# Optimization experiments

Hardware: AMD Instinct MI355X
Metric: run time of the kernel (lower is better)

Reference implementation:

```python
import jax, jax.numpy as jnp
import numpy as np

D_MODEL = 1024
N_HEADS = 16
HEAD_DIM = D_MODEL // N_HEADS
SCALE = HEAD_DIM ** -0.5
NEG = -9e15


def setup_inputs() -> dict:
    key = jax.random.key(0)
    k1, k2, k3 = jax.random.split(key, 3)
    B, S = 4, 2048
    x = jax.random.normal(k1, (B, S, D_MODEL), dtype=jnp.float32)
    W_qkv = jax.random.normal(k2, (D_MODEL, 3 * D_MODEL), dtype=jnp.float32) * (D_MODEL ** -0.5)
    b_qkv = jnp.zeros((3 * D_MODEL,), dtype=jnp.float32)
    W_out = jax.random.normal(k3, (D_MODEL, D_MODEL), dtype=jnp.float32) * (D_MODEL ** -0.5)
    b_out = jnp.zeros((D_MODEL,), dtype=jnp.float32)
    return {"x": x, "W_qkv": W_qkv, "b_qkv": b_qkv, "W_out": W_out, "b_out": b_out}


def reference(x, W_qkv, b_qkv, W_out, b_out):
    B, S, _ = x.shape
    qkv = x @ W_qkv + b_qkv                      # [B,S,3D]
    q, k, v = jnp.split(qkv, 3, axis=-1)
    def heads(t):
        return t.reshape(B, S, N_HEADS, HEAD_DIM).transpose(0, 2, 1, 3)  # [B,H,S,d]
    q, k, v = heads(q), heads(k), heads(v)
    logits = jnp.einsum('bhqd,bhkd->bhqk', q, k) * SCALE
    causal = jnp.tril(jnp.ones((S, S), dtype=bool))
    logits = jnp.where(causal[None, None], logits, jnp.float32(NEG))
    attn = jax.nn.softmax(logits, axis=-1)       # dropout p=0 -> identity
    vals = jnp.einsum('bhqk,bhkd->bhqd', attn, v)
    vals = vals.transpose(0, 2, 1, 3).reshape(B, S, D_MODEL)
    return vals @ W_out + b_out
```

## Files before the change

kernel.cpp:

```cpp
#include <hip/hip_runtime.h>

typedef unsigned short u16;
typedef unsigned int u32;
typedef __attribute__((ext_vector_type(8))) short bf16x8;
typedef __attribute__((ext_vector_type(4))) float f32x4;

#define MFMA16(a, b, c) __builtin_amdgcn_mfma_f32_16x16x32_bf16((a), (b), (c), 0, 0, 0)

constexpr int D = 1024;
constexpr int NH = 16;
constexpr int HD = 64;
constexpr int BB = 4;
constexpr int SS = 2048;
constexpr int BH = BB * NH;
constexpr int MTOK = BB * SS;
constexpr float SCALE_LOG2E = 0.125f * 1.44269504088896340736f;

__device__ __forceinline__ u16 f32_bf16(float f) {
  union { float f; u32 u; } v; v.f = f;
  u32 u = v.u;
  u += 0x7FFFu + ((u >> 16) & 1u);
  return (u16)(u >> 16);
}

__device__ __forceinline__ float exp2_fast(float x) {
  float r; asm("v_exp_f32 %0, %1" : "=v"(r) : "v"(x)); return r;
}
__device__ __forceinline__ u16 cvt_bf16_1(float f) {
  u32 r; asm("v_cvt_pk_bf16_f32 %0, %1, %1" : "=v"(r) : "v"(f)); return (u16)r;
}

__device__ __forceinline__ void gload_lds16(const void* g, u16* l) {
  __builtin_amdgcn_global_load_lds(
      (const __attribute__((address_space(1))) u32*)g,
      (__attribute__((address_space(3))) u32*)l, 16, 0, 0);
}

__global__ __launch_bounds__(256)
void cvt_bf16(const float* __restrict__ in, u16* __restrict__ out, int n4) {
  int i = blockIdx.x * 256 + threadIdx.x;
  const int stride = gridDim.x * 256;
  for (; i < n4; i += stride) {
    float4 v = reinterpret_cast<const float4*>(in)[i];
    u32 lo = (u32)f32_bf16(v.x) | ((u32)f32_bf16(v.y) << 16);
    u32 hi = (u32)f32_bf16(v.z) | ((u32)f32_bf16(v.w) << 16);
    reinterpret_cast<uint2*>(out)[i] = make_uint2(lo, hi);
  }
}

__global__ __launch_bounds__(256)
void transpose_bf16(const float* __restrict__ in, u16* __restrict__ out, int R, int C) {
  __shared__ float tile[32][33];
  const int c0 = blockIdx.x * 32, r0 = blockIdx.y * 32;
  const int tx = threadIdx.x, ty = threadIdx.y;
#pragma unroll
  for (int i = 0; i < 4; i++)
    tile[ty + 8 * i][tx] = in[(size_t)(r0 + ty + 8 * i) * C + c0 + tx];
  __syncthreads();
#pragma unroll
  for (int i = 0; i < 4; i++)
    out[(size_t)(c0 + ty + 8 * i) * R + r0 + tx] = f32_bf16(tile[tx][ty + 8 * i]);
}

template <int MODE>
__global__ __launch_bounds__(256)
void gemm_bf16(const u16* __restrict__ A, const u16* __restrict__ Bt,
               const float* __restrict__ bias,
               u16* __restrict__ q_out, u16* __restrict__ k_out,
               u16* __restrict__ vt_out, float* __restrict__ f_out,
               int M, int N, int K) {
  constexpr int BK = 32;
  __shared__ u16 lds_a[128 * BK];
  __shared__ u16 lds_b[128 * BK];
  const int m0 = blockIdx.x * 128;
  const int n0 = blockIdx.y * 128;
  const int t = threadIdx.x;
  const int lane = t & 63;
  const int w = t >> 6;
  const int wr = w >> 1, wc = w & 1;
  const int fr = lane & 15, fq = lane >> 4;

  const int srow = t >> 2;
  const int schunk = (t & 3) ^ ((srow >> 1) & 3);
  const u16* ga0 = A + (size_t)(m0 + srow) * K + schunk * 8;
  const u16* ga1 = ga0 + (size_t)64 * K;
  const u16* gb0 = Bt + (size_t)(n0 + srow) * K + schunk * 8;
  const u16* gb1 = gb0 + (size_t)64 * K;
  u16* la0 = lds_a + t * 8;
  u16* la1 = lds_a + (t + 256) * 8;
  u16* lb0 = lds_b + t * 8;
  u16* lb1 = lds_b + (t + 256) * 8;

  const int swz = ((fr >> 1) & 3) << 4;
  const char* ca = (const char*)lds_a;
  const char* cb = (const char*)lds_b;

  f32x4 acc[4][4] = {};

  for (int k0 = 0; k0 < K; k0 += BK) {
    __syncthreads();
    gload_lds16(ga0, la0);
    gload_lds16(ga1, la1);
    gload_lds16(gb0, lb0);
    gload_lds16(gb1, lb1);
    ga0 += BK; ga1 += BK; gb0 += BK; gb1 += BK;
    __syncthreads();
    bf16x8 af[4], bfr[4];
#pragma unroll
    for (int i = 0; i < 4; i++)
      af[i] = *reinterpret_cast<const bf16x8*>(
          ca + (wr * 64 + i * 16 + fr) * 64 + ((fq * 16) ^ swz));
#pragma unroll
    for (int i = 0; i < 4; i++)
      bfr[i] = *reinterpret_cast<const bf16x8*>(
          cb + (wc * 64 + i * 16 + fr) * 64 + ((fq * 16) ^ swz));
#pragma unroll
    for (int i = 0; i < 4; i++)
#pragma unroll
      for (int j = 0; j < 4; j++)
        acc[i][j] = MFMA16(af[i], bfr[j], acc[i][j]);
  }

#pragma unroll
  for (int i = 0; i < 4; i++) {
#pragma unroll
    for (int j = 0; j < 4; j++) {
      const int ncol = n0 + wc * 64 + j * 16 + fr;
      const float bs = bias[ncol];
#pragma unroll
      for (int r = 0; r < 4; r++) {
        const int mrow = m0 + wr * 64 + i * 16 + fq * 4 + r;
        const float vv = acc[i][j][r] + bs;
        if (MODE == 0) {
          const int which = ncol >> 10;
          const int rem = ncol & 1023;
          const int hh = rem >> 6, dd = rem & 63;
          const int bb = mrow >> 11, ss = mrow & 2047;
          const int bh = bb * 16 + hh;
          if (which == 0)
            q_out[((size_t)bh * SS + ss) * HD + dd] = f32_bf16(vv * SCALE_LOG2E);
          else if (which == 1)
            k_out[((size_t)bh * SS + ss) * HD + dd] = f32_bf16(vv);
          else
            vt_out[((size_t)bh * HD + dd) * SS + ss] = f32_bf16(vv);
        } else {
          f_out[(size_t)mrow * N + ncol] = vv;
        }
      }
    }
  }
}

__global__ __launch_bounds__(512)
void attn_fwd(const u16* __restrict__ Qb, const u16* __restrict__ Kb,
              const u16* __restrict__ Vt, u16* __restrict__ vals) {
  const int bid = blockIdx.x;
  const int wk = (bid & 7) * 64 + (bid >> 3);
  const int bh = wk >> 3;
  const int pA = wk & 7;
  const int qtA = pA, qtB = 15 - pA;
  const int nA = 2 * qtA + 2;
  const int nTot = 34;
  const u16* Qp = Qb + (size_t)bh * SS * HD;
  const char* Kp = (const char*)(Kb + (size_t)bh * SS * HD);
  const char* Vp = (const char*)(Vt + (size_t)bh * HD * SS);
  const int t = threadIdx.x, lane = t & 63, w = t >> 6;
  const int fr = lane & 15, fq = lane >> 4;
  const int swz = (fr & 7) << 4;

  __shared__ u16 kbuf[3][4096];
  __shared__ u16 vbuf[3][4096];
  __shared__ u16 plds[8][16][72];
  u16* myp = &plds[w][0][0];

  const int lin = t * 16;

  int offKV[8];
#pragma unroll
  for (int kf = 0; kf < 4; kf++)
#pragma unroll
    for (int kk = 0; kk < 2; kk++)
      offKV[kf * 2 + kk] = (kf * 16 + fr) * 128 + ((kk * 64 + fq * 16) ^ swz);

  bf16x8 aq[2];
  {
    const int qbase = qtA * 128 + w * 16;
#pragma unroll
    for (int kk = 0; kk < 2; kk++)
      aq[kk] = *reinterpret_cast<const bf16x8*>(Qp + (size_t)(qbase + fr) * HD + kk * 32 + fq * 8);
  }

  f32x4 o[4] = {};
  float mrun[4], lpart[4];
#pragma unroll
  for (int j = 0; j < 4; j++) { mrun[j] = -3e38f; lpart[j] = 0.f; }

#define STAGE(bufi, kvt_)                                                     \
  {                                                                           \
    const int row = lin >> 7, colb = lin & 127;                               \
    const int scol = colb ^ ((row & 7) << 4);                                 \
    gload_lds16(Kp + (size_t)((kvt_) * 64 + row) * 128 + scol,                \
                &kbuf[bufi][lin >> 1]);                                       \
    gload_lds16(Vp + (size_t)row * 4096 + (kvt_) * 128 + scol,                \
                &vbuf[bufi][lin >> 1]);                                       \
  }
#define KVIDX(ti_) ((ti_) >= nA ? (ti_) - nA : (ti_))

  auto write_out = [&](int qt) {
    const int b_ = bh >> 4, h_ = bh & 15;
    const int qb = qt * 128 + w * 16;
    float linv[4];
#pragma unroll
    for (int j = 0; j < 4; j++) {
      float rs = lpart[j];
#pragma unroll
      for (int off = 1; off < 16; off <<= 1)
        rs += __shfl_xor(rs, off, 64);
      linv[j] = 1.f / rs;
    }
#pragma unroll
    for (int df = 0; df < 4; df++)
#pragma unroll
      for (int j = 0; j < 4; j++) {
        const float vv = o[df][j] * linv[j];
        const int qg = qb + fq * 4 + j;
        vals[((size_t)(b_ * SS + qg)) * D + h_ * HD + df * 16 + fr] = cvt_bf16_1(vv);
      }
  };

  int cur = 0;
  STAGE(0, 0);
  STAGE(1, 1);

  for (int ti = 0; ti < nTot; ++ti) {
    const bool segB = ti >= nA;
    const int kvt = segB ? ti - nA : ti;
    const int qt = segB ? qtB : qtA;

    if (ti + 1 < nTot)
      asm volatile("s_waitcnt vmcnt(2)" ::: "memory");
    else
      asm volatile("s_waitcnt vmcnt(0)" ::: "memory");
    __builtin_amdgcn_s_barrier();
    __builtin_amdgcn_sched_barrier(0);

    if (ti == nA) {
      write_out(qtA);
      const int qbase = qtB * 128 + w * 16;
#pragma unroll
      for (int kk = 0; kk < 2; kk++)
        aq[kk] = *reinterpret_cast<const bf16x8*>(Qp + (size_t)(qbase + fr) * HD + kk * 32 + fq * 8);
#pragma unroll
      for (int j = 0; j < 4; j++) { mrun[j] = -3e38f; lpart[j] = 0.f; }
#pragma unroll
      for (int df = 0; df < 4; df++) o[df] = f32x4{0.f, 0.f, 0.f, 0.f};
    }

    const char* kb = (const char*)kbuf[cur];
    const char* vb = (const char*)vbuf[cur];

    f32x4 sc[4] = {};
    __builtin_amdgcn_s_setprio(1);
#pragma unroll
    for (int kf = 0; kf < 4; kf++) {
#pragma unroll
      for (int kk = 0; kk < 2; kk++) {
        bf16x8 bk = *reinterpret_cast<const bf16x8*>(kb + offKV[kf * 2 + kk]);
        sc[kf] = MFMA16(aq[kk], bk, sc[kf]);
      }
    }
    __builtin_amdgcn_s_setprio(0);
    if ((kvt >> 1) == qt) {
      const int kg0 = kvt * 64 + fr;
      const int rg0 = qt * 128 + w * 16 + fq * 4;
#pragma unroll
      for (int kf = 0; kf < 4; kf++)
#pragma unroll
        for (int j = 0; j < 4; j++)
          if (kg0 + kf * 16 > rg0 + j) sc[kf][j] = -3e38f;
    }
    float mj[4];
#pragma unroll
    for (int j = 0; j < 4; j++) {
      float m = fmaxf(fmaxf(sc[0][j], sc[1][j]), fmaxf(sc[2][j], sc[3][j]));
#pragma unroll
      for (int off = 1; off < 16; off <<= 1)
        m = fmaxf(m, __shfl_xor(m, off, 64));
      mj[j] = m;
    }
    const bool need = (mj[0] > mrun[0] + 8.f) | (mj[1] > mrun[1] + 8.f) |
                      (mj[2] > mrun[2] + 8.f) | (mj[3] > mrun[3] + 8.f);
    if (__any((int)need)) {
#pragma unroll
      for (int j = 0; j < 4; j++) {
        const float mnew = fmaxf(mrun[j], mj[j]);
        const float alpha = exp2_fast(mrun[j] - mnew);
        mrun[j] = mnew;
        lpart[j] *= alpha;
#pragma unroll
        for (int df = 0; df < 4; df++) o[df][j] *= alpha;
      }
    }
#pragma unroll
    for (int j = 0; j < 4; j++) {
#pragma unroll
      for (int kf = 0; kf < 4; kf++) {
        const float p = exp2_fast(sc[kf][j] - mrun[j]);
        sc[kf][j] = p;
        lpart[j] += p;
      }
    }
#pragma unroll
    for (int kf = 0; kf < 4; kf++)
#pragma unroll
      for (int j = 0; j < 4; j++)
        myp[(fq * 4 + j) * 72 + kf * 16 + fr] = cvt_bf16_1(sc[kf][j]);
    bf16x8 pa[2];
#pragma unroll
    for (int kk = 0; kk < 2; kk++)
      pa[kk] = *reinterpret_cast<const bf16x8*>(myp + fr * 72 + kk * 32 + fq * 8);
    __builtin_amdgcn_s_setprio(1);
#pragma unroll
    for (int df = 0; df < 4; df++) {
#pragma unroll
      for (int kk = 0; kk < 2; kk++) {
        bf16x8 bv = *reinterpret_cast<const bf16x8*>(vb + offKV[df * 2 + kk]);
        o[df] = MFMA16(pa[kk], bv, o[df]);
      }
    }
    __builtin_amdgcn_s_setprio(0);

    const int nxt = ti + 2;
    if (nxt < nTot) {
      const int bufn = cur >= 1 ? cur - 1 : 2;
      STAGE(bufn, KVIDX(nxt));
    }
    cur = cur == 2 ? 0 : cur + 1;
  }
  write_out(qtB);
#undef STAGE
#undef KVIDX
}

extern "C" void kernel_launch(void* const* d_in, const int* in_sizes, int n_in,
                              void* d_out, int out_size, void* d_ws, size_t ws_size,
                              hipStream_t stream) {
  const float* x = (const float*)d_in[0];
  const float* Wqkv = (const float*)d_in[1];
  const float* bqkv = (const float*)d_in[2];
  const float* Wout = (const float*)d_in[3];
  const float* bout = (const float*)d_in[4];
  float* out = (float*)d_out;

  char* p = (char*)d_ws;
  u16* xb = (u16*)p;    p += (size_t)MTOK * D * 2;
  u16* wqkvT = (u16*)p; p += (size_t)3 * D * D * 2;
  u16* woutT = (u16*)p; p += (size_t)D * D * 2;
  u16* Qb = (u16*)p;    p += (size_t)BH * SS * HD * 2;
  u16* Kb = (u16*)p;    p += (size_t)BH * SS * HD * 2;
  u16* Vt = (u16*)p;    p += (size_t)BH * SS * HD * 2;
  u16* vals = (u16*)p;  p += (size_t)MTOK * D * 2;

  cvt_bf16<<<2048, 256, 0, stream>>>(x, xb, MTOK * D / 4);
  transpose_bf16<<<dim3(3 * D / 32, D / 32), dim3(32, 8), 0, stream>>>(Wqkv, wqkvT, D, 3 * D);
  transpose_bf16<<<dim3(D / 32, D / 32), dim3(32, 8), 0, stream>>>(Wout, woutT, D, D);
  gemm_bf16<0><<<dim3(MTOK / 128, 3 * D / 128), 256, 0, stream>>>(
      xb, wqkvT, bqkv, Qb, Kb, Vt, nullptr, MTOK, 3 * D, D);
  attn_fwd<<<dim3(512), 512, 0, stream>>>(Qb, Kb, Vt, vals);
  gemm_bf16<1><<<dim3(MTOK / 128, D / 128), 256, 0, stream>>>(
      vals, woutT, bout, nullptr, nullptr, nullptr, out, MTOK, D, D);
}
```

Measured before the change: 204.8 us.

## Double-buffer LDS tiles in bf16 GEMM to overlap global loads with MFMA

```diff
diff --git a/kernel.cpp b/kernel.cpp
--- a/kernel.cpp
+++ b/kernel.cpp
@@ -70,8 +70,8 @@
                u16* __restrict__ vt_out, float* __restrict__ f_out,
                int M, int N, int K) {
   constexpr int BK = 32;
-  __shared__ u16 lds_a[128 * BK];
-  __shared__ u16 lds_b[128 * BK];
+  __shared__ u16 lds_a[2][128 * BK];
+  __shared__ u16 lds_b[2][128 * BK];
   const int m0 = blockIdx.x * 128;
   const int n0 = blockIdx.y * 128;
   const int t = threadIdx.x;
@@ -86,25 +86,29 @@
   const u16* ga1 = ga0 + (size_t)64 * K;
   const u16* gb0 = Bt + (size_t)(n0 + srow) * K + schunk * 8;
   const u16* gb1 = gb0 + (size_t)64 * K;
-  u16* la0 = lds_a + t * 8;
-  u16* la1 = lds_a + (t + 256) * 8;
-  u16* lb0 = lds_b + t * 8;
-  u16* lb1 = lds_b + (t + 256) * 8;
 
   const int swz = ((fr >> 1) & 3) << 4;
-  const char* ca = (const char*)lds_a;
-  const char* cb = (const char*)lds_b;
+
+#define GSTAGE(bufi, koff)                                                    \
+  {                                                                           \
+    gload_lds16(ga0 + (koff), lds_a[bufi] + t * 8);                           \
+    gload_lds16(ga1 + (koff), lds_a[bufi] + (t + 256) * 8);                   \
+    gload_lds16(gb0 + (koff), lds_b[bufi] + t * 8);                           \
+    gload_lds16(gb1 + (koff), lds_b[bufi] + (t + 256) * 8);                   \
+  }
 
   f32x4 acc[4][4] = {};
 
+  GSTAGE(0, 0);
+  asm volatile("s_waitcnt vmcnt(0)" ::: "memory");
+  __builtin_amdgcn_s_barrier();
+
+  int cur = 0;
   for (int k0 = 0; k0 < K; k0 += BK) {
-    __syncthreads();
-    gload_lds16(ga0, la0);
-    gload_lds16(ga1, la1);
-    gload_lds16(gb0, lb0);
-    gload_lds16(gb1, lb1);
-    ga0 += BK; ga1 += BK; gb0 += BK; gb1 += BK;
-    __syncthreads();
+    if (k0 + BK < K) GSTAGE(cur ^ 1, k0 + BK);
+
+    const char* ca = (const char*)lds_a[cur];
+    const char* cb = (const char*)lds_b[cur];
     bf16x8 af[4], bfr[4];
 #pragma unroll
     for (int i = 0; i < 4; i++)
@@ -114,12 +118,20 @@
     for (int i = 0; i < 4; i++)
       bfr[i] = *reinterpret_cast<const bf16x8*>(
           cb + (wc * 64 + i * 16 + fr) * 64 + ((fq * 16) ^ swz));
+    __builtin_amdgcn_s_setprio(1);
 #pragma unroll
     for (int i = 0; i < 4; i++)
 #pragma unroll
       for (int j = 0; j < 4; j++)
         acc[i][j] = MFMA16(af[i], bfr[j], acc[i][j]);
-  }
+    __builtin_amdgcn_s_setprio(0);
+
+    asm volatile("s_waitcnt vmcnt(0)" ::: "memory");
+    __builtin_amdgcn_s_barrier();
+    __builtin_amdgcn_sched_barrier(0);
+    cur ^= 1;
+  }
+#undef GSTAGE
 
 #pragma unroll
   for (int i = 0; i < 4; i++) {
```

Result: faster. 196.3 us (-4.2%).
